# Kernel tuning notes

Hardware: AMD Instinct MI355X
Metric: run time of the kernel (lower is better)

## Reference

```python
import jax, jax.numpy as jnp
import numpy as np


def _graph_conv(feat_src, e_src, e_dst, n_src, n_dst, W, b):
    # DGL GraphConv, norm='both', bipartite block; feat_src: [N_src, A, C, H]
    ones_e = jnp.ones(e_src.shape[0], dtype=feat_src.dtype)
    out_deg = jax.ops.segment_sum(ones_e, e_src, num_segments=n_src)
    in_deg = jax.ops.segment_sum(ones_e, e_dst, num_segments=n_dst)
    norm_src = jnp.clip(out_deg, 1.0) ** -0.5
    norm_dst = jnp.clip(in_deg, 1.0) ** -0.5
    feat = feat_src * norm_src[:, None, None, None]
    # in_feats == out_feats -> DGL multiplies by W before aggregation
    feat = jnp.einsum('nach,ho->naco', feat, W)
    msgs = feat[e_src]                                   # gather  [E, A, C, H]
    agg = jax.ops.segment_sum(msgs, e_dst, num_segments=n_dst)  # scatter-add
    return agg * norm_dst[:, None, None, None] + b


def setup_inputs() -> dict:
    key = jax.random.key(0)
    ks = jax.random.split(key, 8)
    H = 128
    N_SRC0, N_DST0, N_DST1 = 50000, 20000, 4096
    E0, E1 = 320000, 65536
    return {
        'in_feat': jax.random.normal(ks[0], (2, H, 2, N_SRC0), dtype=jnp.float32),
        'W': jax.random.normal(ks[1], (H, H), dtype=jnp.float32) / np.sqrt(H),
        'b': jnp.zeros((H,), dtype=jnp.float32),
        'e0_src': jax.random.randint(ks[2], (E0,), 0, N_SRC0, dtype=jnp.int32),
        'e0_dst': jax.random.randint(ks[3], (E0,), 0, N_DST0, dtype=jnp.int32),
        'e1_src': jax.random.randint(ks[4], (E1,), 0, N_DST0, dtype=jnp.int32),
        'e1_dst': jax.random.randint(ks[5], (E1,), 0, N_DST1, dtype=jnp.int32),
        'n_dst0': N_DST0,
        'n_dst1': N_DST1,
    }


def reference(in_feat, W, b, e0_src, e0_dst, e1_src, e1_dst, n_dst0, n_dst1):
    # [A, H, C, N] -> [N, A, C, H]
    x = jnp.transpose(in_feat, (3, 0, 2, 1))
    n_src0 = x.shape[0]
    h = _graph_conv(x, e0_src, e0_dst, n_src0, n_dst0, W, b)
    h = jax.nn.relu(h)
    h = _graph_conv(h, e1_src, e1_dst, n_dst0, n_dst1, W, b)
    h = jax.nn.relu(h)
    # [N_dst1, A, C, H] -> [A, H, C, N_dst1]
    out = jnp.transpose(h, (1, 3, 2, 0))
    return jax.nn.relu(out)
```

## Files before the change

kernel.cpp:

```cpp
#include <hip/hip_runtime.h>
#include <math.h>

#define H128 128
#define NF 512
typedef unsigned short u16;

__device__ inline u16 f2bf(float f) {
  union { float f; unsigned u; } x; x.f = f;
  unsigned r = x.u + 0x7FFFu + ((x.u >> 16) & 1u);
  return (u16)(r >> 16);
}
__device__ inline void addbf8(float* a, uint4 u) {
  a[0] += __uint_as_float(u.x << 16);
  a[1] += __uint_as_float(u.x & 0xFFFF0000u);
  a[2] += __uint_as_float(u.y << 16);
  a[3] += __uint_as_float(u.y & 0xFFFF0000u);
  a[4] += __uint_as_float(u.z << 16);
  a[5] += __uint_as_float(u.z & 0xFFFF0000u);
  a[6] += __uint_as_float(u.w << 16);
  a[7] += __uint_as_float(u.w & 0xFFFF0000u);
}

__global__ void k_count4(const int* __restrict__ e0s, const int* __restrict__ e0d,
                         const int* __restrict__ e1s, const int* __restrict__ e1d,
                         int E0, int E1,
                         int* __restrict__ c_s0, int* __restrict__ c_d0,
                         int* __restrict__ c_s1, int* __restrict__ c_d1) {
  int i = blockIdx.x * 256 + threadIdx.x;
  if (i < E0) { atomicAdd(&c_s0[e0s[i]], 1); return; }
  i -= E0;
  if (i < E0) { atomicAdd(&c_d0[e0d[i]], 1); return; }
  i -= E0;
  if (i < E1) { atomicAdd(&c_s1[e1s[i]], 1); return; }
  i -= E1;
  if (i < E1) { atomicAdd(&c_d1[e1d[i]], 1); }
}

__global__ void k_norm(int* __restrict__ buf, int n) {
  int i = blockIdx.x * 256 + threadIdx.x;
  if (i < n) {
    int d = buf[i];
    float dv = (d < 1) ? 1.0f : (float)d;
    ((float*)buf)[i] = 1.0f / sqrtf(dv);
  }
}

__global__ void k_scan2(const int* __restrict__ degA, int nA, int* __restrict__ offA, int* __restrict__ curA,
                        const int* __restrict__ degB, int nB, int* __restrict__ offB, int* __restrict__ curB) {
  const int* deg = blockIdx.x ? degB : degA;
  int n = blockIdx.x ? nB : nA;
  int* off = blockIdx.x ? offB : offA;
  int* cur = blockIdx.x ? curB : curA;
  __shared__ int wsum[16];
  const int tid = threadIdx.x;
  const int lane = tid & 63;
  const int wv = tid >> 6;
  const int per = (n + 1023) >> 10;
  const int base = tid * per;
  int cnt = n - base;
  if (cnt < 0) cnt = 0;
  if (cnt > per) cnt = per;
  int sum = 0;
  for (int i = 0; i < cnt; ++i) sum += deg[base + i];
  int x = sum;
  #pragma unroll
  for (int d2 = 1; d2 < 64; d2 <<= 1) {
    int y = __shfl_up(x, (unsigned)d2, 64);
    if (lane >= d2) x += y;
  }
  if (lane == 63) wsum[wv] = x;
  __syncthreads();
  if (wv == 0 && lane < 16) {
    int w = wsum[lane];
    #pragma unroll
    for (int d2 = 1; d2 < 16; d2 <<= 1) {
      int y = __shfl_up(w, (unsigned)d2, 64);
      if (lane >= d2) w += y;
    }
    wsum[lane] = w;
  }
  __syncthreads();
  int tbase = x - sum + (wv ? wsum[wv - 1] : 0);
  int running = tbase;
  for (int i = 0; i < cnt; ++i) {
    off[base + i] = running;
    cur[base + i] = running;
    running += deg[base + i];
  }
  if (tid == 1023) off[n] = wsum[15];
}

__global__ void k_scatter2(const int* __restrict__ e0s, const int* __restrict__ e0d,
                           const int* __restrict__ e1s, const int* __restrict__ e1d,
                           int E0, int E1,
                           int* __restrict__ cur0, int* __restrict__ csr0,
                           int* __restrict__ cur1, int* __restrict__ csr1) {
  int i = blockIdx.x * 256 + threadIdx.x;
  if (i < E0) {
    int p = atomicAdd(&cur0[e0d[i]], 1);
    csr0[p] = e0s[i];
    return;
  }
  i -= E0;
  if (i < E1) {
    int p = atomicAdd(&cur1[e1d[i]], 1);
    csr1[p] = e1s[i];
  }
}

__global__ __launch_bounds__(256) void k_transpose_in(
    const float* __restrict__ in, const float* __restrict__ norm,
    u16* __restrict__ xp, int N) {
  __shared__ float tile[64 * 128];
  const int tid = threadIdx.x;
  const int n0 = blockIdx.x << 6;
  const int ac = blockIdx.y;
  const int a = ac >> 1, c = ac & 1;
  const float* base = in + ((size_t)a * 256 + c) * (size_t)N;
  #pragma unroll
  for (int i = 0; i < 8; ++i) {
    int fidx = (i << 8) + tid;
    int h = fidx >> 4;
    int n = (fidx & 15) << 2;
    int gn = n0 + n;
    float4 v = make_float4(0.f, 0.f, 0.f, 0.f);
    if (gn < N) v = *(const float4*)(base + (size_t)h * 2 * N + gn);
    int q = h >> 2, rem = h & 3;
    tile[(n + 0) * 128 + (((q + n + 0) & 31) << 2) + rem] = v.x;
    tile[(n + 1) * 128 + (((q + n + 1) & 31) << 2) + rem] = v.y;
    tile[(n + 2) * 128 + (((q + n + 2) & 31) << 2) + rem] = v.z;
    tile[(n + 3) * 128 + (((q + n + 3) & 31) << 2) + rem] = v.w;
  }
  __syncthreads();
  #pragma unroll
  for (int i = 0; i < 8; ++i) {
    int fidx = (i << 8) + tid;
    int h4 = fidx & 31;
    int n = fidx >> 5;
    int gn = n0 + n;
    if (gn < N) {
      float4 v = *(const float4*)(&tile[n * 128 + (((h4 + n) & 31) << 2)]);
      float s = norm[gn];
      ushort4 o;
      o.x = f2bf(v.x * s); o.y = f2bf(v.y * s);
      o.z = f2bf(v.z * s); o.w = f2bf(v.w * s);
      *(ushort4*)(xp + (size_t)gn * NF + ac * H128 + (h4 << 2)) = o;
    }
  }
}

__global__ __launch_bounds__(256) void k_agg(
    const u16* __restrict__ xp, const int* __restrict__ csr,
    const int* __restrict__ off, const float* __restrict__ norm_dst,
    u16* __restrict__ outp, int ndst) {
  const int wave = threadIdx.x >> 6;
  const int lane = threadIdx.x & 63;
  const int d = blockIdx.x * 4 + wave;
  if (d >= ndst) return;
  const int s = off[d], e = off[d + 1];
  float acc[8];
  #pragma unroll
  for (int i = 0; i < 8; ++i) acc[i] = 0.f;
  int j = s;
  for (; j + 4 <= e; j += 4) {
    int s0 = csr[j], s1 = csr[j + 1], s2 = csr[j + 2], s3 = csr[j + 3];
    uint4 u0 = *((const uint4*)(xp + (size_t)s0 * NF) + lane);
    uint4 u1 = *((const uint4*)(xp + (size_t)s1 * NF) + lane);
    uint4 u2 = *((const uint4*)(xp + (size_t)s2 * NF) + lane);
    uint4 u3 = *((const uint4*)(xp + (size_t)s3 * NF) + lane);
    addbf8(acc, u0); addbf8(acc, u1); addbf8(acc, u2); addbf8(acc, u3);
  }
  for (; j < e; ++j) {
    uint4 u = *((const uint4*)(xp + (size_t)csr[j] * NF) + lane);
    addbf8(acc, u);
  }
  float nd = norm_dst[d];
  u16* orow = outp + (size_t)d * NF + lane * 8;
  ushort4 o0, o1;
  o0.x = f2bf(acc[0] * nd); o0.y = f2bf(acc[1] * nd);
  o0.z = f2bf(acc[2] * nd); o0.w = f2bf(acc[3] * nd);
  o1.x = f2bf(acc[4] * nd); o1.y = f2bf(acc[5] * nd);
  o1.z = f2bf(acc[6] * nd); o1.w = f2bf(acc[7] * nd);
  *(ushort4*)orow = o0;
  *(ushort4*)(orow + 4) = o1;
}

template <int BR, int RT, bool OUT_BF16>
__global__ __launch_bounds__(256) void k_gemm(
    const u16* __restrict__ A, const float* __restrict__ W,
    const float* __restrict__ bias, const float* __restrict__ scale,
    void* __restrict__ outv, int M) {
  __shared__ float As[32][BR + 4];
  __shared__ float Ws[32][132];
  const int tid = threadIdx.x;
  const int tx = tid & 15;
  const int ty = tid >> 4;
  const int c0 = tx << 2;
  const int row0 = blockIdx.x * BR;
  float acc[RT][8];
  #pragma unroll
  for (int r = 0; r < RT; ++r)
    #pragma unroll
    for (int c = 0; c < 8; ++c) acc[r][c] = 0.f;

  for (int kc = 0; kc < 128; kc += 32) {
    __syncthreads();
    #pragma unroll
    for (int i = 0; i < 4; ++i) {
      int fidx = (i << 8) + tid;
      int k = fidx >> 5, cq = fidx & 31;
      *(float4*)(&Ws[k][cq << 2]) = *(const float4*)(W + (size_t)(kc + k) * 128 + (cq << 2));
    }
    #pragma unroll
    for (int i = 0; i < BR / 64; ++i) {
      int fidx = (i << 8) + tid;
      int r = fidx >> 2, c8 = fidx & 3;
      int row = row0 + r;
      uint4 u = make_uint4(0u, 0u, 0u, 0u);
      if (row < M) u = *(const uint4*)(A + (size_t)row * 128 + kc + (c8 << 3));
      int k = c8 << 3;
      As[k + 0][r] = __uint_as_float(u.x << 16);
      As[k + 1][r] = __uint_as_float(u.x & 0xFFFF0000u);
      As[k + 2][r] = __uint_as_float(u.y << 16);
      As[k + 3][r] = __uint_as_float(u.y & 0xFFFF0000u);
      As[k + 4][r] = __uint_as_float(u.z << 16);
      As[k + 5][r] = __uint_as_float(u.z & 0xFFFF0000u);
      As[k + 6][r] = __uint_as_float(u.w << 16);
      As[k + 7][r] = __uint_as_float(u.w & 0xFFFF0000u);
    }
    __syncthreads();
    #pragma unroll 4
    for (int k = 0; k < 32; ++k) {
      float4 w0 = *(const float4*)(&Ws[k][c0]);
      float4 w1 = *(const float4*)(&Ws[k][64 + c0]);
      float a[RT];
      #pragma unroll
      for (int rr = 0; rr < RT / 4; ++rr) {
        float4 av = *(const float4*)(&As[k][ty * RT + (rr << 2)]);
        a[rr * 4 + 0] = av.x; a[rr * 4 + 1] = av.y;
        a[rr * 4 + 2] = av.z; a[rr * 4 + 3] = av.w;
      }
      #pragma unroll
      for (int r = 0; r < RT; ++r) {
        acc[r][0] = fmaf(a[r], w0.x, acc[r][0]);
        acc[r][1] = fmaf(a[r], w0.y, acc[r][1]);
        acc[r][2] = fmaf(a[r], w0.z, acc[r][2]);
        acc[r][3] = fmaf(a[r], w0.w, acc[r][3]);
        acc[r][4] = fmaf(a[r], w1.x, acc[r][4]);
        acc[r][5] = fmaf(a[r], w1.y, acc[r][5]);
        acc[r][6] = fmaf(a[r], w1.z, acc[r][6]);
        acc[r][7] = fmaf(a[r], w1.w, acc[r][7]);
      }
    }
  }
  float4 b0 = *(const float4*)(bias + c0);
  float4 b1 = *(const float4*)(bias + 64 + c0);
  #pragma unroll
  for (int r = 0; r < RT; ++r) {
    int row = row0 + ty * RT + r;
    if (row < M) {
      float sc = scale ? scale[row >> 2] : 1.f;
      float v[8];
      v[0] = acc[r][0] + b0.x; v[1] = acc[r][1] + b0.y;
      v[2] = acc[r][2] + b0.z; v[3] = acc[r][3] + b0.w;
      v[4] = acc[r][4] + b1.x; v[5] = acc[r][5] + b1.y;
      v[6] = acc[r][6] + b1.z; v[7] = acc[r][7] + b1.w;
      #pragma unroll
      for (int c = 0; c < 8; ++c) v[c] = (v[c] > 0.f ? v[c] : 0.f) * sc;
      if (OUT_BF16) {
        u16* out = (u16*)outv;
        ushort4 q0, q1;
        q0.x = f2bf(v[0]); q0.y = f2bf(v[1]); q0.z = f2bf(v[2]); q0.w = f2bf(v[3]);
        q1.x = f2bf(v[4]); q1.y = f2bf(v[5]); q1.z = f2bf(v[6]); q1.w = f2bf(v[7]);
        *(ushort4*)(out + (size_t)row * 128 + c0) = q0;
        *(ushort4*)(out + (size_t)row * 128 + 64 + c0) = q1;
      } else {
        float* out = (float*)outv;
        *(float4*)(out + (size_t)row * 128 + c0) = make_float4(v[0], v[1], v[2], v[3]);
        *(float4*)(out + (size_t)row * 128 + 64 + c0) = make_float4(v[4], v[5], v[6], v[7]);
      }
    }
  }
}

__global__ __launch_bounds__(256) void k_transpose_out(
    const float* __restrict__ h1, float* __restrict__ out, int N) {
  __shared__ float tile[128][68];
  const int tid = threadIdx.x;
  const int n0 = blockIdx.x << 6;
  const int ac = blockIdx.y;
  const int a = ac >> 1, c = ac & 1;
  #pragma unroll
  for (int i = 0; i < 8; ++i) {
    int fidx = (i << 8) + tid;
    int h4 = fidx & 31;
    int n = fidx >> 5;
    float4 v = *(const float4*)(h1 + (size_t)(n0 + n) * NF + ac * H128 + (h4 << 2));
    int h = h4 << 2;
    tile[h + 0][n] = v.x; tile[h + 1][n] = v.y;
    tile[h + 2][n] = v.z; tile[h + 3][n] = v.w;
  }
  __syncthreads();
  float* obase = out + ((size_t)a * 256 + c) * (size_t)N;
  #pragma unroll
  for (int i = 0; i < 8; ++i) {
    int fidx = (i << 8) + tid;
    int h = fidx >> 4;
    int n = (fidx & 15) << 2;
    float4 v = *(const float4*)(&tile[h][n]);
    *(float4*)(obase + (size_t)h * 2 * N + n0 + n) = v;
  }
}

extern "C" void kernel_launch(void* const* d_in, const int* in_sizes, int n_in,
                              void* d_out, int out_size, void* d_ws, size_t ws_size,
                              hipStream_t stream) {
  const float* in_feat = (const float*)d_in[0];
  const float* W       = (const float*)d_in[1];
  const float* bias    = (const float*)d_in[2];
  const int* e0_src    = (const int*)d_in[3];
  const int* e0_dst    = (const int*)d_in[4];
  const int* e1_src    = (const int*)d_in[5];
  const int* e1_dst    = (const int*)d_in[6];
  const int N_DST0 = 20000;
  const int N_DST1 = 4096;
  const int N_SRC0 = in_sizes[0] / NF;
  const int E0 = in_sizes[3];
  const int E1 = in_sizes[5];

  u16* xp    = (u16*)d_ws;
  u16* h0    = xp + (size_t)N_SRC0 * NF;
  u16* agg0b = h0 + (size_t)N_DST0 * NF;
  u16* agg1b = agg0b + (size_t)N_DST0 * NF;
  float* h1  = (float*)(agg1b + (size_t)N_DST1 * NF);
  int* ibase    = (int*)(h1 + (size_t)N_DST1 * NF);
  int* cnt_src0 = ibase;
  int* cnt_dst0 = cnt_src0 + N_SRC0;
  int* cnt_src1 = cnt_dst0 + N_DST0;
  int* cnt_dst1 = cnt_src1 + N_DST0;
  int* off0 = cnt_dst1 + N_DST1;
  int* cur0 = off0 + N_DST0 + 1;
  int* csr0 = cur0 + N_DST0;
  int* off1 = csr0 + E0;
  int* cur1 = off1 + N_DST1 + 1;
  int* csr1 = cur1 + N_DST1;

  const int NCNT = N_SRC0 + N_DST0 + N_DST0 + N_DST1;
  hipMemsetAsync(cnt_src0, 0, (size_t)NCNT * sizeof(int), stream);

  int tot_cnt = 2 * E0 + 2 * E1;
  k_count4<<<(tot_cnt + 255) / 256, 256, 0, stream>>>(
      e0_src, e0_dst, e1_src, e1_dst, E0, E1, cnt_src0, cnt_dst0, cnt_src1, cnt_dst1);

  k_scan2<<<2, 1024, 0, stream>>>(cnt_dst0, N_DST0, off0, cur0,
                                  cnt_dst1, N_DST1, off1, cur1);

  k_norm<<<(NCNT + 255) / 256, 256, 0, stream>>>(cnt_src0, NCNT);

  k_scatter2<<<(E0 + E1 + 255) / 256, 256, 0, stream>>>(
      e0_src, e0_dst, e1_src, e1_dst, E0, E1, cur0, csr0, cur1, csr1);

  dim3 tg1((N_SRC0 + 63) / 64, 4);
  k_transpose_in<<<tg1, 256, 0, stream>>>(in_feat, (const float*)cnt_src0, xp, N_SRC0);

  k_agg<<<(N_DST0 + 3) / 4, 256, 0, stream>>>(
      xp, csr0, off0, (const float*)cnt_dst0, agg0b, N_DST0);
  k_gemm<128, 8, true><<<(N_DST0 * 4) / 128, 256, 0, stream>>>(
      agg0b, W, bias, (const float*)cnt_src1, (void*)h0, N_DST0 * 4);

  k_agg<<<(N_DST1 + 3) / 4, 256, 0, stream>>>(
      h0, csr1, off1, (const float*)cnt_dst1, agg1b, N_DST1);
  k_gemm<64, 4, false><<<(N_DST1 * 4) / 64, 256, 0, stream>>>(
      agg1b, W, bias, nullptr, (void*)h1, N_DST1 * 4);

  dim3 tg2(N_DST1 / 64, 4);
  k_transpose_out<<<tg2, 256, 0, stream>>>(h1, (float*)d_out, N_DST1);
}
```

Measured before the change: 394.2 us.

## Replace FP32 SIMT GEMMs with bf16 MFMA using prepacked weight fragments

Both 128x128 weight GEMMs now use the bf16 16x16x32 MFMA instruction instead of a shared-memory FP32 FMA tiling loop. A new small kernel packs W into bf16 MFMA B-operand fragments once per call, and each GEMM block copies them into LDS. Each wave handles 16 rows, loading its A fragments straight from global memory. This rounds W to bf16, which adds precision loss. The epilogue writes scalar elements instead of vectorised stores, and there is one extra launch.

```diff
diff --git a/kernel.cpp b/kernel.cpp
--- a/kernel.cpp
+++ b/kernel.cpp
@@ -4,6 +4,8 @@
 #define H128 128
 #define NF 512
 typedef unsigned short u16;
+typedef __attribute__((ext_vector_type(8))) short short8;
+typedef __attribute__((ext_vector_type(4))) float floatx4;
 
 __device__ inline u16 f2bf(float f) {
   union { float f; unsigned u; } x; x.f = f;
@@ -108,6 +110,19 @@
   }
 }
 
+__global__ void k_wfrag(const float* __restrict__ W, uint4* __restrict__ wfrag) {
+  int t = blockIdx.x * 256 + threadIdx.x;
+  int lane = t & 63;
+  int pair = t >> 6;
+  int ct = pair >> 2, kc = pair & 3;
+  int quad = lane >> 4, r = lane & 15;
+  const float* src = W + (size_t)(kc * 32 + quad * 8) * 128 + ct * 16 + r;
+  union { u16 v[8]; uint4 u; } pk;
+  #pragma unroll
+  for (int j = 0; j < 8; ++j) pk.v[j] = f2bf(src[(size_t)j * 128]);
+  wfrag[t] = pk.u;
+}
+
 __global__ __launch_bounds__(256) void k_transpose_in(
     const float* __restrict__ in, const float* __restrict__ norm,
     u16* __restrict__ xp, int N) {
@@ -185,100 +200,48 @@
   *(ushort4*)(orow + 4) = o1;
 }
 
-template <int BR, int RT, bool OUT_BF16>
-__global__ __launch_bounds__(256) void k_gemm(
-    const u16* __restrict__ A, const float* __restrict__ W,
+template <bool OUT_BF16>
+__global__ __launch_bounds__(256) void k_gemm_mfma(
+    const u16* __restrict__ A, const uint4* __restrict__ wfrag,
     const float* __restrict__ bias, const float* __restrict__ scale,
     void* __restrict__ outv, int M) {
-  __shared__ float As[32][BR + 4];
-  __shared__ float Ws[32][132];
+  __shared__ uint4 wb[2048];
   const int tid = threadIdx.x;
-  const int tx = tid & 15;
-  const int ty = tid >> 4;
-  const int c0 = tx << 2;
-  const int row0 = blockIdx.x * BR;
-  float acc[RT][8];
-  #pragma unroll
-  for (int r = 0; r < RT; ++r)
+  #pragma unroll
+  for (int i = 0; i < 8; ++i) wb[i * 256 + tid] = wfrag[i * 256 + tid];
+  __syncthreads();
+  const int wave = tid >> 6;
+  const int lane = tid & 63;
+  const int quad = lane >> 4;
+  const int r = lane & 15;
+  const int row0 = (blockIdx.x * 4 + wave) << 4;
+  if (row0 >= M) return;
+  short8 a[4];
+  const u16* abase = A + (size_t)(row0 + r) * 128 + quad * 8;
+  #pragma unroll
+  for (int kc = 0; kc < 4; ++kc) a[kc] = *(const short8*)(abase + kc * 32);
+  floatx4 acc[8];
+  #pragma unroll
+  for (int ct = 0; ct < 8; ++ct) acc[ct] = (floatx4){0.f, 0.f, 0.f, 0.f};
+  #pragma unroll
+  for (int kc = 0; kc < 4; ++kc) {
     #pragma unroll
-    for (int c = 0; c < 8; ++c) acc[r][c] = 0.f;
-
-  for (int kc = 0; kc < 128; kc += 32) {
-    __syncthreads();
+    for (int ct = 0; ct < 8; ++ct) {
+      short8 b = *(const short8*)&wb[(ct * 4 + kc) * 64 + lane];
+      acc[ct] = __builtin_amdgcn_mfma_f32_16x16x32_bf16(a[kc], b, acc[ct], 0, 0, 0);
+    }
+  }
+  float sc = scale ? scale[(row0 >> 2) + quad] : 1.f;
+  #pragma unroll
+  for (int ct = 0; ct < 8; ++ct) {
+    float bcol = bias[ct * 16 + r];
     #pragma unroll
-    for (int i = 0; i < 4; ++i) {
-      int fidx = (i << 8) + tid;
-      int k = fidx >> 5, cq = fidx & 31;
-      *(float4*)(&Ws[k][cq << 2]) = *(const float4*)(W + (size_t)(kc + k) * 128 + (cq << 2));
-    }
-    #pragma unroll
-    for (int i = 0; i < BR / 64; ++i) {
-      int fidx = (i << 8) + tid;
-      int r = fidx >> 2, c8 = fidx & 3;
-      int row = row0 + r;
-      uint4 u = make_uint4(0u, 0u, 0u, 0u);
-      if (row < M) u = *(const uint4*)(A + (size_t)row * 128 + kc + (c8 << 3));
-      int k = c8 << 3;
-      As[k + 0][r] = __uint_as_float(u.x << 16);
-      As[k + 1][r] = __uint_as_float(u.x & 0xFFFF0000u);
-      As[k + 2][r] = __uint_as_float(u.y << 16);
-      As[k + 3][r] = __uint_as_float(u.y & 0xFFFF0000u);
-      As[k + 4][r] = __uint_as_float(u.z << 16);
-      As[k + 5][r] = __uint_as_float(u.z & 0xFFFF0000u);
-      As[k + 6][r] = __uint_as_float(u.w << 16);
-      As[k + 7][r] = __uint_as_float(u.w & 0xFFFF0000u);
-    }
-    __syncthreads();
-    #pragma unroll 4
-    for (int k = 0; k < 32; ++k) {
-      float4 w0 = *(const float4*)(&Ws[k][c0]);
-      float4 w1 = *(const float4*)(&Ws[k][64 + c0]);
-      float a[RT];
-      #pragma unroll
-      for (int rr = 0; rr < RT / 4; ++rr) {
-        float4 av = *(const float4*)(&As[k][ty * RT + (rr << 2)]);
-        a[rr * 4 + 0] = av.x; a[rr * 4 + 1] = av.y;
-        a[rr * 4 + 2] = av.z; a[rr * 4 + 3] = av.w;
-      }
-      #pragma unroll
-      for (int r = 0; r < RT; ++r) {
-        acc[r][0] = fmaf(a[r], w0.x, acc[r][0]);
-        acc[r][1] = fmaf(a[r], w0.y, acc[r][1]);
-        acc[r][2] = fmaf(a[r], w0.z, acc[r][2]);
-        acc[r][3] = fmaf(a[r], w0.w, acc[r][3]);
-        acc[r][4] = fmaf(a[r], w1.x, acc[r][4]);
-        acc[r][5] = fmaf(a[r], w1.y, acc[r][5]);
-        acc[r][6] = fmaf(a[r], w1.z, acc[r][6]);
-        acc[r][7] = fmaf(a[r], w1.w, acc[r][7]);
-      }
-    }
-  }
-  float4 b0 = *(const float4*)(bias + c0);
-  float4 b1 = *(const float4*)(bias + 64 + c0);
-  #pragma unroll
-  for (int r = 0; r < RT; ++r) {
-    int row = row0 + ty * RT + r;
-    if (row < M) {
-      float sc = scale ? scale[row >> 2] : 1.f;
-      float v[8];
-      v[0] = acc[r][0] + b0.x; v[1] = acc[r][1] + b0.y;
-      v[2] = acc[r][2] + b0.z; v[3] = acc[r][3] + b0.w;
-      v[4] = acc[r][4] + b1.x; v[5] = acc[r][5] + b1.y;
-      v[6] = acc[r][6] + b1.z; v[7] = acc[r][7] + b1.w;
-      #pragma unroll
-      for (int c = 0; c < 8; ++c) v[c] = (v[c] > 0.f ? v[c] : 0.f) * sc;
-      if (OUT_BF16) {
-        u16* out = (u16*)outv;
-        ushort4 q0, q1;
-        q0.x = f2bf(v[0]); q0.y = f2bf(v[1]); q0.z = f2bf(v[2]); q0.w = f2bf(v[3]);
-        q1.x = f2bf(v[4]); q1.y = f2bf(v[5]); q1.z = f2bf(v[6]); q1.w = f2bf(v[7]);
-        *(ushort4*)(out + (size_t)row * 128 + c0) = q0;
-        *(ushort4*)(out + (size_t)row * 128 + 64 + c0) = q1;
-      } else {
-        float* out = (float*)outv;
-        *(float4*)(out + (size_t)row * 128 + c0) = make_float4(v[0], v[1], v[2], v[3]);
-        *(float4*)(out + (size_t)row * 128 + 64 + c0) = make_float4(v[4], v[5], v[6], v[7]);
-      }
+    for (int reg = 0; reg < 4; ++reg) {
+      float v = acc[ct][reg] + bcol;
+      v = (v > 0.f ? v : 0.f) * sc;
+      size_t idx = (size_t)(row0 + quad * 4 + reg) * 128 + ct * 16 + r;
+      if (OUT_BF16) ((u16*)outv)[idx] = f2bf(v);
+      else          ((float*)outv)[idx] = v;
     }
   }
 }
@@ -344,6 +307,7 @@
   int* off1 = csr0 + E0;
   int* cur1 = off1 + N_DST1 + 1;
   int* csr1 = cur1 + N_DST1;
+  uint4* wfrag = (uint4*)(((uintptr_t)(csr1 + E1) + 15) & ~(uintptr_t)15);
 
   const int NCNT = N_SRC0 + N_DST0 + N_DST0 + N_DST1;
   hipMemsetAsync(cnt_src0, 0, (size_t)NCNT * sizeof(int), stream);
@@ -360,18 +324,20 @@
   k_scatter2<<<(E0 + E1 + 255) / 256, 256, 0, stream>>>(
       e0_src, e0_dst, e1_src, e1_dst, E0, E1, cur0, csr0, cur1, csr1);
 
+  k_wfrag<<<8, 256, 0, stream>>>(W, wfrag);
+
   dim3 tg1((N_SRC0 + 63) / 64, 4);
   k_transpose_in<<<tg1, 256, 0, stream>>>(in_feat, (const float*)cnt_src0, xp, N_SRC0);
 
   k_agg<<<(N_DST0 + 3) / 4, 256, 0, stream>>>(
       xp, csr0, off0, (const float*)cnt_dst0, agg0b, N_DST0);
-  k_gemm<128, 8, true><<<(N_DST0 * 4) / 128, 256, 0, stream>>>(
-      agg0b, W, bias, (const float*)cnt_src1, (void*)h0, N_DST0 * 4);
+  k_gemm_mfma<true><<<(N_DST0 * 4) / 64, 256, 0, stream>>>(
+      agg0b, wfrag, bias, (const float*)cnt_src1, (void*)h0, N_DST0 * 4);
 
   k_agg<<<(N_DST1 + 3) / 4, 256, 0, stream>>>(
       h0, csr1, off1, (const float*)cnt_dst1, agg1b, N_DST1);
-  k_gemm<64, 4, false><<<(N_DST1 * 4) / 64, 256, 0, stream>>>(
-      agg1b, W, bias, nullptr, (void*)h1, N_DST1 * 4);
+  k_gemm_mfma<false><<<(N_DST1 * 4) / 64, 256, 0, stream>>>(
+      agg1b, wfrag, bias, nullptr, (void*)h1, N_DST1 * 4);
 
   dim3 tg2(N_DST1 / 64, 4);
   k_transpose_out<<<tg2, 256, 0, stream>>>(h1, (float*)d_out, N_DST1);
```

After: 357.6 us. 1.1x faster.
